# Performance work log

Hardware: AMD Instinct MI355X
Metric: run time of the kernel (lower is better)

The kernel has to match this reference:

```python
import jax, jax.numpy as jnp
import numpy as np

N, F, H, E, ES, G = 50000, 64, 4, 300000, 400000, 128
NS, EPS = 0.2, 1e-5  # LeakyReLU slope, BN eps


def setup_inputs() -> dict:
    k = jax.random.split(jax.random.key(0), 16)
    rn = lambda i, s, sc=1.0: jax.random.normal(k[i], s, jnp.float32) * sc
    return {
        "x": rn(0, (N, F)),
        "edge_index": jax.random.randint(k[1], (2, E), 0, N),
        "batch": jnp.sort(jax.random.randint(k[2], (N,), 0, G)),
        "scatter_edge_index": jax.random.randint(k[3], (4, 2, ES), 0, N),
        "scatter_edge_attr": rn(4, (4, ES), 0.1),
        "gat_W": rn(5, (4, F, H * F), 0.05),
        "gat_asrc": rn(6, (4, H, F), 0.05),
        "gat_adst": rn(7, (4, H, F), 0.05),
        "gat_bias": jnp.zeros((4, H * F)),
        "mlp_W": rn(8, (4, H * F, F), 0.05),
        "mlp_b": jnp.zeros((4, F)),
        "mlp_g": jnp.ones((4, F)), "mlp_beta": jnp.zeros((4, F)),
        "mlp_rm": jnp.zeros((4, F)), "mlp_rv": jax.random.uniform(k[9], (4, F)) + 0.5,
        "fc1_W": rn(10, (F, 256), 0.05), "fc1_b": jnp.zeros((256,)),
        "fc1_g": jnp.ones((256,)), "fc1_beta": jnp.zeros((256,)),
        "fc1_rm": jnp.zeros((256,)), "fc1_rv": jax.random.uniform(k[11], (256,)) + 0.5,
        "fc2_W": rn(12, (256, 64), 0.05), "fc2_b": jnp.zeros((64,)),
        "fc2_g": jnp.ones((64,)), "fc2_beta": jnp.zeros((64,)),
        "fc2_rm": jnp.zeros((64,)), "fc2_rv": jax.random.uniform(k[13], (64,)) + 0.5,
        "fc3_W": rn(14, (64, 10), 0.05), "fc3_b": jnp.zeros((10,)),
        "fc3_g": jnp.ones((10,)), "fc3_beta": jnp.zeros((10,)),
        "fc3_rm": jnp.zeros((10,)), "fc3_rv": jax.random.uniform(k[15], (10,)) + 0.5,
    }


def _bn(h, g, b, rm, rv):
    # BatchNorm1d in eval mode (running stats)
    return g * (h - rm) * jax.lax.rsqrt(rv + EPS) + b


def _forward(floats, ints):
    (x, sea, gW, gas, gad, gb, mW, mb, mg, mbe, mrm, mrv,
     f1W, f1b, f1g, f1be, f1rm, f1rv, f2W, f2b, f2g, f2be, f2rm, f2rv,
     f3W, f3b, f3g, f3be, f3rm, f3rv) = floats
    edge_index, batch, sei = ints
    n = x.shape[0]
    loop = jnp.arange(n)
    src = jnp.concatenate([edge_index[0], loop])  # GATConv adds self-loops
    dst = jnp.concatenate([edge_index[1], loop])

    def solo(i, h):
        # edge_attr-weighted scatter-add (solo_pass, aggr='add')
        s, t = sei[i, 0], sei[i, 1]
        return jax.ops.segment_sum(sea[i][:, None] * h[s], t, num_segments=n)

    def gat_mlp(i, h):
        hh = (h @ gW[i]).reshape(n, H, F)                       # [N,H,F]
        e = (hh * gas[i]).sum(-1)[src] + (hh * gad[i]).sum(-1)[dst]  # [E+N,H]
        e = jnp.where(e > 0, e, NS * e)                         # LeakyReLU(0.2)
        m = jax.ops.segment_max(e, dst, num_segments=n)         # segment softmax over dst
        ex = jnp.exp(e - m[dst])
        ssum = jax.ops.segment_sum(ex, dst, num_segments=n)
        alpha = ex / ssum[dst]
        out = jax.ops.segment_sum(hh[src] * alpha[:, :, None], dst, num_segments=n)
        out = out.reshape(n, H * F) + gb[i]                     # concat heads + bias
        h2 = jax.nn.elu(out) @ mW[i] + mb[i]                    # ELU -> Dropout(eval) -> Linear
        return _bn(h2, mg[i], mbe[i], mrm[i], mrv[i])

    x0 = solo(0, x)
    xh = [jnp.abs(solo(i, x)) for i in (1, 2, 3)]
    branches = [x0] + [solo(0, h) for h in xh]
    branches = [gat_mlp(i, branches[i]) for i in range(4)]
    x_stage2 = x + branches[0] + branches[1] + branches[2] + branches[3]
    pooled = jax.ops.segment_sum(x_stage2, batch, num_segments=G)   # global_add_pool
    h = jax.nn.relu(_bn(pooled @ f1W + f1b, f1g, f1be, f1rm, f1rv))
    h = jax.nn.relu(_bn(h @ f2W + f2b, f2g, f2be, f2rm, f2rv))
    return _bn(h @ f3W + f3b, f3g, f3be, f3rm, f3rv)  # [G, num_classes]


def reference(x, edge_index, batch, scatter_edge_index, scatter_edge_attr, gat_W, gat_asrc, gat_adst, gat_bias, mlp_W, mlp_b, mlp_g, mlp_beta, mlp_rm, mlp_rv, fc1_W, fc1_b, fc1_g, fc1_beta, fc1_rm, fc1_rv, fc2_W, fc2_b, fc2_g, fc2_beta, fc2_rm, fc2_rv, fc3_W, fc3_b, fc3_g, fc3_beta, fc3_rm, fc3_rv):
    floats = (x, scatter_edge_attr, gat_W, gat_asrc, gat_adst, gat_bias, mlp_W, mlp_b, mlp_g, mlp_beta, mlp_rm, mlp_rv, fc1_W, fc1_b, fc1_g, fc1_beta, fc1_rm, fc1_rv, fc2_W, fc2_b, fc2_g, fc2_beta, fc2_rm, fc2_rv, fc3_W, fc3_b, fc3_g, fc3_beta, fc3_rm, fc3_rv)
    return _forward(floats, (edge_index, batch, scatter_edge_index))
```

## Files before the change

kernel.cpp:

```cpp
#include <hip/hip_runtime.h>

typedef unsigned int uint;

#define NN 50000
#define FF 64
#define NHD 4
#define EE 300000
#define ESN 400000
#define NG 128
#define NSLOPE 0.2f
#define EPSBN 1e-5f
#define NTILE 3125

#define BINSZ 64
#define NBIN 782
#define CHUNK 2048
#define NBLK 196
#define BST 40
#define BCAP 38

typedef float f32x4 __attribute__((ext_vector_type(4)));
typedef float f32x2 __attribute__((ext_vector_type(2)));
typedef short bf16x8 __attribute__((ext_vector_type(8)));
union U8 { uint4 u; bf16x8 s; };

static __device__ __forceinline__ float lrelu(float e) {
  return fmaxf(e, NSLOPE * e);
}
static __device__ __forceinline__ float bl(uint u) {
  return __uint_as_float(u << 16);
}
static __device__ __forceinline__ float bh(uint u) {
  return __uint_as_float(u & 0xFFFF0000u);
}
static __device__ __forceinline__ uint f2bf(float f) {
  uint u = __float_as_uint(f);
  return (u + 0x7FFFu + ((u >> 16) & 1u)) >> 16;
}
static __device__ __forceinline__ uint packbf(float a, float b) {
  return f2bf(a) | (f2bf(b) << 16);
}

__global__ __launch_bounds__(256) void k_setup(
    const float2* __restrict__ x, const float* __restrict__ gW,
    const float* __restrict__ gas, const float* __restrict__ gad,
    const float* __restrict__ mW, const float* __restrict__ mb,
    const float* __restrict__ mg, const float* __restrict__ mbe,
    const float* __restrict__ mrm, const float* __restrict__ mrv,
    uint* __restrict__ xbf, uint* __restrict__ WB, uint* __restrict__ SB,
    uint* __restrict__ MB, float* __restrict__ cvec) {
  int i = blockIdx.x * 256 + threadIdx.x;
  if (i < NN * 32) {
    float2 v = x[i];
    xbf[i] = packbf(v.x, v.y);
  }
  int t = i;
  if (t < 8192) {
    int b = t >> 11, rem = t & 2047;
    int tt = rem >> 6, l = rem & 63;
    int tile = tt >> 1, q2 = tt & 1;
    int c = tile * 16 + (l & 15);
    int k0 = q2 * 32 + (l >> 4) * 8;
    const float* Wp = gW + b * 16384;
    uint4 o;
    o.x = packbf(Wp[(k0 + 0) * 256 + c], Wp[(k0 + 1) * 256 + c]);
    o.y = packbf(Wp[(k0 + 2) * 256 + c], Wp[(k0 + 3) * 256 + c]);
    o.z = packbf(Wp[(k0 + 4) * 256 + c], Wp[(k0 + 5) * 256 + c]);
    o.w = packbf(Wp[(k0 + 6) * 256 + c], Wp[(k0 + 7) * 256 + c]);
    ((uint4*)WB)[t] = o;
  } else if (t < 8192 + 2048) {
    int id = t - 8192;
    int b = id >> 9, rem = id & 511;
    int q2 = rem >> 6, l = rem & 63;
    int n = l & 15;
    int k0 = q2 * 32 + (l >> 4) * 8;
    const float* ap = gas + b * 256;
    const float* dp = gad + b * 256;
    float v[8];
#pragma unroll
    for (int j = 0; j < 8; ++j) {
      int c = k0 + j, h = c >> 6, f = c & 63;
      float val = 0.f;
      if (n < 4) val = (h == n) ? ap[n * 64 + f] : 0.f;
      else if (n < 8) val = (h == n - 4) ? dp[(n - 4) * 64 + f] : 0.f;
      v[j] = val;
    }
    uint4 o;
    o.x = packbf(v[0], v[1]); o.y = packbf(v[2], v[3]);
    o.z = packbf(v[4], v[5]); o.w = packbf(v[6], v[7]);
    ((uint4*)SB)[id] = o;
  } else if (t < 8192 + 2048 + 8192) {
    int id = t - 10240;
    int b = id >> 11, rem = id & 2047;
    int tt = rem >> 6, l = rem & 63;
    int tile = tt >> 3, q2 = tt & 7;
    int c = tile * 16 + (l & 15);
    int k0 = q2 * 32 + (l >> 4) * 8;
    const float* Mp = mW + b * 16384;
    float sc = mg[b * 64 + c] * rsqrtf(mrv[b * 64 + c] + EPSBN);
    float v[8];
#pragma unroll
    for (int j = 0; j < 8; ++j) {
      int kp = k0 + j;
      int ko = (kp & 3) * 64 + (kp >> 2);
      v[j] = Mp[ko * 64 + c] * sc;
    }
    uint4 o;
    o.x = packbf(v[0], v[1]); o.y = packbf(v[2], v[3]);
    o.z = packbf(v[4], v[5]); o.w = packbf(v[6], v[7]);
    ((uint4*)MB)[id] = o;
  } else if (t < 8192 + 2048 + 8192 + 64) {
    int c = t - 18432;
    float acc = 0.f;
#pragma unroll
    for (int b = 0; b < 4; ++b) {
      float sc = mg[b * 64 + c] * rsqrtf(mrv[b * 64 + c] + EPSBN);
      acc += sc * (mb[b * 64 + c] - mrm[b * 64 + c]) + mbe[b * 64 + c];
    }
    cvec[c] = acc;
  }
}

__global__ __launch_bounds__(256) void k_sort1(
    const int* __restrict__ sei, const float* __restrict__ sea,
    const int* __restrict__ ei, uint2* __restrict__ sorted,
    unsigned short* __restrict__ offs) {
  __shared__ uint hist[NBIN];
  __shared__ uint wsum[4];
  __shared__ __align__(16) uint2 buf[CHUNK];
  int y = blockIdx.y, blk = blockIdx.x, tid = threadIdx.x;
  int E = (y < 4) ? ESN : EE;
  int e0 = blk * CHUNK;
  if (e0 >= E) return;
  int ec = E - e0; if (ec > CHUNK) ec = CHUNK;
  for (int i = tid; i < NBIN; i += 256) hist[i] = 0;
  __syncthreads();
  const int* sptr; const int* tptr; const float* wptr = 0;
  if (y < 4) {
    sptr = sei + (size_t)y * 2 * ESN; tptr = sptr + ESN;
    wptr = sea + (size_t)y * ESN;
  } else {
    sptr = ei; tptr = ei + EE;
  }
  uint2 rec[8]; uint rbin[8];
#pragma unroll
  for (int k = 0; k < 8; ++k) {
    int idx = tid + k * 256;
    rbin[k] = 0xFFFFFFFFu;
    if (idx < ec) {
      int e = e0 + idx;
      int s = sptr[e], t = tptr[e];
      uint w = (y < 4) ? (f2bf(wptr[e]) << 16) : 0u;
      rec[k].x = (uint)s | ((uint)(t & 63) << 16);
      rec[k].y = w;
      rbin[k] = (uint)(t >> 6);
      atomicAdd(&hist[rbin[k]], 1u);
    }
  }
  __syncthreads();
  int t4 = tid * 4;
  uint h0 = 0, h1 = 0, h2 = 0, h3 = 0;
  if (t4 + 0 < NBIN) h0 = hist[t4 + 0];
  if (t4 + 1 < NBIN) h1 = hist[t4 + 1];
  if (t4 + 2 < NBIN) h2 = hist[t4 + 2];
  if (t4 + 3 < NBIN) h3 = hist[t4 + 3];
  uint sl = h0 + h1 + h2 + h3;
  uint pre = sl;
#pragma unroll
  for (int off = 1; off < 64; off <<= 1) {
    uint nv = __shfl_up(pre, off);
    if ((tid & 63) >= off) pre += nv;
  }
  int wid = tid >> 6;
  if ((tid & 63) == 63) wsum[wid] = pre;
  __syncthreads();
  uint wbase = 0;
#pragma unroll
  for (int w = 0; w < 4; ++w) if (w < wid) wbase += wsum[w];
  uint base = wbase + pre - sl;
  if (t4 + 0 < NBIN) hist[t4 + 0] = base;
  if (t4 + 1 < NBIN) hist[t4 + 1] = base + h0;
  if (t4 + 2 < NBIN) hist[t4 + 2] = base + h0 + h1;
  if (t4 + 3 < NBIN) hist[t4 + 3] = base + h0 + h1 + h2;
  __syncthreads();
  unsigned short* ob = offs + ((size_t)y * NBLK + blk) * 784;
  for (int i = tid; i < NBIN; i += 256) ob[i] = (unsigned short)hist[i];
  if (tid == 0) { ob[NBIN] = (unsigned short)ec; ob[NBIN + 1] = (unsigned short)ec; }
  __syncthreads();
#pragma unroll
  for (int k = 0; k < 8; ++k) {
    if (rbin[k] != 0xFFFFFFFFu) {
      uint p = atomicAdd(&hist[rbin[k]], 1u);
      buf[p] = rec[k];
    }
  }
  __syncthreads();
  uint2* sb = sorted + ((size_t)y * NBLK + blk) * CHUNK;
  uint4* s4 = (uint4*)sb;
  const uint4* b4 = (const uint4*)buf;
  int n4 = (ec + 1) >> 1;
  for (int i = tid; i < n4; i += 256) s4[i] = b4[i];
}

__global__ __launch_bounds__(256) void k_sort2(
    const unsigned short* __restrict__ offs, const uint2* __restrict__ sorted,
    uint* __restrict__ pbk, uint* __restrict__ gbk) {
  __shared__ __align__(16) uint Lb[BINSZ * BST];
  __shared__ uint Lc[BINSZ];
  int y = blockIdx.y, bin = blockIdx.x, tid = threadIdx.x;
  if (tid < BINSZ) Lc[tid] = 0u;
  __syncthreads();
  int nblk = (y < 4) ? NBLK : 147;
  for (int sb = tid; sb < nblk; sb += 256) {
    const unsigned short* ob = offs + ((size_t)y * NBLK + sb) * 784;
    uint st = ob[bin], en = ob[bin + 1];
    const uint2* src = sorted + ((size_t)y * NBLK + sb) * CHUNK;
    for (uint i = st; i < en; ++i) {
      uint2 r = src[i];
      uint tl = (r.x >> 16) & 63u;
      uint p = atomicAdd(&Lc[tl], 1u);
      if (p < BCAP) Lb[tl * BST + 2 + p] = (r.x & 0xFFFFu) | r.y;
    }
  }
  __syncthreads();
  if (tid < BINSZ) Lb[tid * BST] = Lc[tid];
  __syncthreads();
  int n0 = bin * BINSZ;
  int nodes = NN - n0;
  if (nodes > BINSZ) nodes = BINSZ;
  uint* out = (y < 4) ? (pbk + ((size_t)y * NN + n0) * BST)
                      : (gbk + (size_t)n0 * BST);
  int tot4 = nodes * (BST / 4);
  uint4* o4v = (uint4*)out;
  const uint4* L4 = (const uint4*)Lb;
  for (int i = tid; i < tot4; i += 256) o4v[i] = L4[i];
}

__global__ __launch_bounds__(256) void k_solo_gA(
    const uint* __restrict__ xbf, const uint* __restrict__ pbk,
    uint* __restrict__ bbuf, uint* __restrict__ tmpb) {
  int i = blockIdx.y;
  int tid = threadIdx.x;
  int n = blockIdx.x * 32 + (tid >> 3);
  int sl = tid & 7;
  if (n >= NN) return;
  const uint* bk = pbk + ((size_t)i * NN + n) * BST;
  int deg = (int)bk[0]; deg = deg > BCAP ? BCAP : deg;
  const uint* pp = bk + 2;
  f32x2 A0 = {0.f, 0.f}, A1 = {0.f, 0.f}, A2 = {0.f, 0.f}, A3 = {0.f, 0.f};
  f32x2 B0 = {0.f, 0.f}, B1 = {0.f, 0.f}, B2 = {0.f, 0.f}, B3 = {0.f, 0.f};
  for (int j = 0; j < deg; j += 2) {
    uint2 pe2 = *(const uint2*)&pp[j];
    if (j + 1 >= deg) pe2.y = 0u;
    float w0 = bh(pe2.x), w1 = bh(pe2.y);
    f32x2 w20 = {w0, w0}, w21 = {w1, w1};
    uint4 v0 = *(const uint4*)&xbf[(size_t)(pe2.x & 0xFFFFu) * 32 + sl * 4];
    uint4 v1 = *(const uint4*)&xbf[(size_t)(pe2.y & 0xFFFFu) * 32 + sl * 4];
    A0 += (f32x2){bl(v0.x), bh(v0.x)} * w20;
    A1 += (f32x2){bl(v0.y), bh(v0.y)} * w20;
    A2 += (f32x2){bl(v0.z), bh(v0.z)} * w20;
    A3 += (f32x2){bl(v0.w), bh(v0.w)} * w20;
    B0 += (f32x2){bl(v1.x), bh(v1.x)} * w21;
    B1 += (f32x2){bl(v1.y), bh(v1.y)} * w21;
    B2 += (f32x2){bl(v1.z), bh(v1.z)} * w21;
    B3 += (f32x2){bl(v1.w), bh(v1.w)} * w21;
  }
  A0 += B0; A1 += B1; A2 += B2; A3 += B3;
  uint4 o;
  o.x = packbf(A0[0], A0[1]); o.y = packbf(A1[0], A1[1]);
  o.z = packbf(A2[0], A2[1]); o.w = packbf(A3[0], A3[1]);
  uint* out = (i == 0) ? bbuf : (tmpb + (size_t)(i - 1) * NN * 32);
  *(uint4*)&out[(size_t)n * 32 + sl * 4] = o;
}

__global__ __launch_bounds__(256) void k_solo_gB(
    const uint* __restrict__ tmpb, const uint* __restrict__ pbk,
    uint* __restrict__ bbuf) {
  int j0 = blockIdx.y;
  int tid = threadIdx.x;
  int n = blockIdx.x * 32 + (tid >> 3);
  int sl = tid & 7;
  if (n >= NN) return;
  const uint* bk = pbk + (size_t)n * BST;
  int deg = (int)bk[0]; deg = deg > BCAP ? BCAP : deg;
  const uint* pp = bk + 2;
  const uint* tin = tmpb + (size_t)j0 * NN * 32;
  f32x2 A0 = {0.f, 0.f}, A1 = {0.f, 0.f}, A2 = {0.f, 0.f}, A3 = {0.f, 0.f};
  f32x2 B0 = {0.f, 0.f}, B1 = {0.f, 0.f}, B2 = {0.f, 0.f}, B3 = {0.f, 0.f};
  for (int j = 0; j < deg; j += 2) {
    uint2 pe2 = *(const uint2*)&pp[j];
    if (j + 1 >= deg) pe2.y = 0u;
    float w0 = bh(pe2.x), w1 = bh(pe2.y);
    f32x2 w20 = {w0, w0}, w21 = {w1, w1};
    uint4 v0 = *(const uint4*)&tin[(size_t)(pe2.x & 0xFFFFu) * 32 + sl * 4];
    uint4 v1 = *(const uint4*)&tin[(size_t)(pe2.y & 0xFFFFu) * 32 + sl * 4];
    A0 += (f32x2){fabsf(bl(v0.x)), fabsf(bh(v0.x))} * w20;
    A1 += (f32x2){fabsf(bl(v0.y)), fabsf(bh(v0.y))} * w20;
    A2 += (f32x2){fabsf(bl(v0.z)), fabsf(bh(v0.z))} * w20;
    A3 += (f32x2){fabsf(bl(v0.w)), fabsf(bh(v0.w))} * w20;
    B0 += (f32x2){fabsf(bl(v1.x)), fabsf(bh(v1.x))} * w21;
    B1 += (f32x2){fabsf(bl(v1.y)), fabsf(bh(v1.y))} * w21;
    B2 += (f32x2){fabsf(bl(v1.z)), fabsf(bh(v1.z))} * w21;
    B3 += (f32x2){fabsf(bl(v1.w)), fabsf(bh(v1.w))} * w21;
  }
  A0 += B0; A1 += B1; A2 += B2; A3 += B3;
  uint4 o;
  o.x = packbf(A0[0], A0[1]); o.y = packbf(A1[0], A1[1]);
  o.z = packbf(A2[0], A2[1]); o.w = packbf(A3[0], A3[1]);
  *(uint4*)&bbuf[(size_t)(j0 + 1) * NN * 32 + (size_t)n * 32 + sl * 4] = o;
}

#define GST 260
__global__ __launch_bounds__(256) void k_gemm_all(
    const uint* __restrict__ bbuf, const uint* __restrict__ WB4,
    const uint* __restrict__ SB4, uint* __restrict__ hh4,
    float* __restrict__ es4, float* __restrict__ ed4) {
  __shared__ float lds[4][16 * GST];
  int b = blockIdx.y;
  const uint* bbuf_i = bbuf + (size_t)b * NN * 32;
  const uint4* WBb = (const uint4*)WB4 + b * 2048;
  const uint4* SBb = (const uint4*)SB4 + b * 512;
  uint* hh = hh4 + (size_t)b * NN * 128;
  float* es = es4 + (size_t)b * NN * 4;
  float* ed = ed4 + (size_t)b * NN * 4;
  int tid = threadIdx.x, wv = tid >> 6, l = tid & 63;
  int quad = l >> 4, m = l & 15;
  int tile = blockIdx.x * 4 + wv;
  if (tile >= NTILE) return;
  int base = tile * 16;
  U8 B[32];
#pragma unroll
  for (int tt = 0; tt < 32; ++tt) B[tt].u = WBb[tt * 64 + l];
  U8 S[8];
#pragma unroll
  for (int q2 = 0; q2 < 8; ++q2) S[q2].u = SBb[q2 * 64 + l];
  U8 a0, a1;
  a0.u = *(const uint4*)&bbuf_i[(size_t)(base + m) * 32 + quad * 4];
  a1.u = *(const uint4*)&bbuf_i[(size_t)(base + m) * 32 + 16 + quad * 4];
  float* L = lds[wv];
#pragma unroll
  for (int t = 0; t < 16; ++t) {
    f32x4 acc = {0.f, 0.f, 0.f, 0.f};
    acc = __builtin_amdgcn_mfma_f32_16x16x32_bf16(a0.s, B[t * 2].s, acc, 0, 0, 0);
    acc = __builtin_amdgcn_mfma_f32_16x16x32_bf16(a1.s, B[t * 2 + 1].s, acc, 0, 0, 0);
#pragma unroll
    for (int r = 0; r < 4; ++r) L[(quad * 4 + r) * GST + t * 16 + m] = acc[r];
  }
  f32x4 accS = {0.f, 0.f, 0.f, 0.f};
#pragma unroll
  for (int q2 = 0; q2 < 8; ++q2) {
    int k0 = q2 * 32 + quad * 8;
    float4 lo = *(const float4*)&L[m * GST + k0];
    float4 hi = *(const float4*)&L[m * GST + k0 + 4];
    U8 af;
    af.u.x = packbf(lo.x, lo.y); af.u.y = packbf(lo.z, lo.w);
    af.u.z = packbf(hi.x, hi.y); af.u.w = packbf(hi.z, hi.w);
    accS = __builtin_amdgcn_mfma_f32_16x16x32_bf16(af.s, S[q2].s, accS, 0, 0, 0);
  }
#pragma unroll
  for (int r = 0; r < 4; ++r) {
    int node = base + quad * 4 + r;
    if (m < 4) es[node * 4 + m] = accS[r];
    else if (m < 8) ed[node * 4 + (m - 4)] = accS[r];
  }
  for (int n = 0; n < 16; ++n) {
    float v0 = L[n * GST + l];
    float v1 = L[n * GST + 64 + l];
    float v2 = L[n * GST + 128 + l];
    float v3 = L[n * GST + 192 + l];
    uint2 o;
    o.x = packbf(v0, v1); o.y = packbf(v2, v3);
    *(uint2*)&hh[(size_t)(base + n) * 128 + l * 2] = o;
  }
}

__global__ __launch_bounds__(256) void k_attn_all(
    const uint* __restrict__ gbk, const float* __restrict__ es4,
    const float* __restrict__ ed4, const uint* __restrict__ hh4,
    const float* __restrict__ gb, uint* __restrict__ att4) {
  __shared__ uint4 meta[4][2][32];
  int b = blockIdx.y;
  const float4* es44 = (const float4*)(es4 + (size_t)b * NN * 4);
  const float4* ed44 = (const float4*)(ed4 + (size_t)b * NN * 4);
  const char* hhB = (const char*)(hh4 + (size_t)b * NN * 128);
  const float* gbb = gb + b * 256;
  uint* att = att4 + (size_t)b * NN * 128;
  int wv = threadIdx.x >> 6, lane = threadIdx.x & 63;
  int half = lane >> 5, hl = lane & 31;
  int d = blockIdx.x * 8 + wv * 2 + half;
  int deg = (int)gbk[(size_t)d * BST]; deg = deg > 31 ? 31 : deg;
  float4 edd = ed44[d];
  bool act = hl <= deg;
  int s0 = d;
  if (hl < deg) s0 = (int)gbk[(size_t)d * BST + 2 + hl];
  float4 e4 = es44[s0];
  float val[4];
  val[0] = act ? lrelu(e4.x + edd.x) : -3e38f;
  val[1] = act ? lrelu(e4.y + edd.y) : -3e38f;
  val[2] = act ? lrelu(e4.z + edd.z) : -3e38f;
  val[3] = act ? lrelu(e4.w + edd.w) : -3e38f;
  float m[4] = {val[0], val[1], val[2], val[3]};
#pragma unroll
  for (int off = 1; off < 32; off <<= 1)
#pragma unroll
    for (int h = 0; h < 4; ++h) m[h] = fmaxf(m[h], __shfl_xor(m[h], off));
  float e[4], sm[4];
#pragma unroll
  for (int h = 0; h < 4; ++h) {
    e[h] = act ? __expf(val[h] - m[h]) : 0.f;
    sm[h] = e[h];
  }
#pragma unroll
  for (int off = 1; off < 32; off <<= 1)
#pragma unroll
    for (int h = 0; h < 4; ++h) sm[h] += __shfl_xor(sm[h], off);
  meta[wv][half][hl] =
      make_uint4((uint)s0 * 512u, packbf(e[0] / sm[0], e[1] / sm[1]),
                 packbf(e[2] / sm[2], e[3] / sm[3]), 0u);
  int tot = deg + 1;
  f32x2 A0 = {0.f, 0.f}, A1 = {0.f, 0.f}, A2 = {0.f, 0.f}, A3 = {0.f, 0.f};
  f32x2 B0 = {0.f, 0.f}, B1 = {0.f, 0.f}, B2 = {0.f, 0.f}, B3 = {0.f, 0.f};
  int passes = (tot + 1) >> 1;
  for (int p = 0; p < passes; ++p) {
    uint4 ma = meta[wv][half][2 * p];
    uint4 mb_ = meta[wv][half][2 * p + 1];
    uint4 r0 = *(const uint4*)(hhB + ma.x + hl * 16);
    uint4 r1 = *(const uint4*)(hhB + mb_.x + hl * 16);
    f32x2 wA0 = {bl(ma.y), bh(ma.y)}, wB0 = {bl(ma.z), bh(ma.z)};
    f32x2 wA1 = {bl(mb_.y), bh(mb_.y)}, wB1 = {bl(mb_.z), bh(mb_.z)};
    A0 += (f32x2){bl(r0.x), bh(r0.x)} * wA0;
    A1 += (f32x2){bl(r0.y), bh(r0.y)} * wB0;
    A2 += (f32x2){bl(r0.z), bh(r0.z)} * wA0;
    A3 += (f32x2){bl(r0.w), bh(r0.w)} * wB0;
    B0 += (f32x2){bl(r1.x), bh(r1.x)} * wA1;
    B1 += (f32x2){bl(r1.y), bh(r1.y)} * wB1;
    B2 += (f32x2){bl(r1.z), bh(r1.z)} * wA1;
    B3 += (f32x2){bl(r1.w), bh(r1.w)} * wB1;
  }
  A0 += B0; A1 += B1; A2 += B2; A3 += B3;
  float ov[8] = {A0[0], A0[1], A1[0], A1[1], A2[0], A2[1], A3[0], A3[1]};
#pragma unroll
  for (int k = 0; k < 8; ++k) {
    float g = gbb[(k & 3) * 64 + hl * 2 + (k >> 2)];
    float v = ov[k] + g;
    ov[k] = v > 0.f ? v : (__expf(v) - 1.f);
  }
  uint4 o;
  o.x = packbf(ov[0], ov[1]); o.y = packbf(ov[2], ov[3]);
  o.z = packbf(ov[4], ov[5]); o.w = packbf(ov[6], ov[7]);
  *(uint4*)&att[(size_t)d * 128 + hl * 4] = o;
}

#define MST 68
__global__ __launch_bounds__(256) void k_mlp_all(
    const uint* __restrict__ att4, const uint* __restrict__ MB4,
    const float* __restrict__ cvec, const float* __restrict__ xsrc,
    float* __restrict__ xs2) {
  __shared__ float lds[4][16 * MST];
  int tid = threadIdx.x, wv = tid >> 6, l = tid & 63;
  int quad = l >> 4, m = l & 15;
  int tile = blockIdx.x * 4 + wv;
  if (tile >= NTILE) return;
  int base = tile * 16;
  f32x4 acc[4] = {{0.f, 0.f, 0.f, 0.f},
                  {0.f, 0.f, 0.f, 0.f},
                  {0.f, 0.f, 0.f, 0.f},
                  {0.f, 0.f, 0.f, 0.f}};
  for (int b = 0; b < 4; ++b) {
    const uint4* MBb = (const uint4*)MB4 + b * 2048;
    const uint* att = att4 + (size_t)b * NN * 128;
    U8 B[32];
#pragma unroll
    for (int tt = 0; tt < 32; ++tt) B[tt].u = MBb[tt * 64 + l];
    U8 A[8];
#pragma unroll
    for (int q2 = 0; q2 < 8; ++q2)
      A[q2].u =
          *(const uint4*)&att[(size_t)(base + m) * 128 + q2 * 16 + quad * 4];
#pragma unroll
    for (int t = 0; t < 4; ++t)
#pragma unroll
      for (int q2 = 0; q2 < 8; ++q2)
        acc[t] = __builtin_amdgcn_mfma_f32_16x16x32_bf16(A[q2].s,
                                                         B[t * 8 + q2].s,
                                                         acc[t], 0, 0, 0);
  }
  float* L = lds[wv];
#pragma unroll
  for (int t = 0; t < 4; ++t)
#pragma unroll
    for (int r = 0; r < 4; ++r) L[(quad * 4 + r) * MST + t * 16 + m] = acc[t][r];
  float cv = cvec[l];
  for (int n = 0; n < 16; ++n) {
    float v = L[n * MST + l];
    size_t idx = (size_t)(base + n) * 64 + l;
    xs2[idx] = xsrc[idx] + v + cv;
  }
}

__global__ __launch_bounds__(256) void k_poolhead(
    const float* __restrict__ xs2, const int* __restrict__ batch,
    const float* __restrict__ f1W, const float* __restrict__ f1b,
    const float* __restrict__ f1g, const float* __restrict__ f1be,
    const float* __restrict__ f1rm, const float* __restrict__ f1rv,
    const float* __restrict__ f2W, const float* __restrict__ f2b,
    const float* __restrict__ f2g, const float* __restrict__ f2be,
    const float* __restrict__ f2rm, const float* __restrict__ f2rv,
    const float* __restrict__ f3W, const float* __restrict__ f3b,
    const float* __restrict__ f3g, const float* __restrict__ f3be,
    const float* __restrict__ f3rm, const float* __restrict__ f3rv,
    float* __restrict__ out) {
  __shared__ float p[64], h1[256], h2[64], red[4][64];
  int g = blockIdx.x, tid = threadIdx.x;
  int wv = tid >> 6, lane = tid & 63;
  int lo = 0, hi = NN;
  while (lo < hi) { int mid = (lo + hi) >> 1; if (batch[mid] < g) lo = mid + 1; else hi = mid; }
  int beg = lo;
  lo = 0; hi = NN;
  while (lo < hi) { int mid = (lo + hi) >> 1; if (batch[mid] < g + 1) lo = mid + 1; else hi = mid; }
  int end = lo;
  float acc = 0.f;
  for (int n = beg + wv; n < end; n += 4) acc += xs2[(size_t)n * FF + lane];
  red[wv][lane] = acc;
  __syncthreads();
  if (tid < 64) p[tid] = red[0][tid] + red[1][tid] + red[2][tid] + red[3][tid];
  __syncthreads();
  {
    float a = f1b[tid];
    for (int k = 0; k < 64; ++k) a += p[k] * f1W[k * 256 + tid];
// ... 26 lines not shown
  const float* sea   = (const float*)d_in[4];
  const float* gW    = (const float*)d_in[5];
  const float* gas   = (const float*)d_in[6];
  const float* gad   = (const float*)d_in[7];
  const float* gb    = (const float*)d_in[8];
  const float* mW    = (const float*)d_in[9];
  const float* mb    = (const float*)d_in[10];
  const float* mg    = (const float*)d_in[11];
  const float* mbe   = (const float*)d_in[12];
  const float* mrm   = (const float*)d_in[13];
  const float* mrv   = (const float*)d_in[14];
  const float* f1W   = (const float*)d_in[15];
  const float* f1b   = (const float*)d_in[16];
  const float* f1g   = (const float*)d_in[17];
  const float* f1be  = (const float*)d_in[18];
  const float* f1rm  = (const float*)d_in[19];
  const float* f1rv  = (const float*)d_in[20];
  const float* f2W   = (const float*)d_in[21];
  const float* f2b   = (const float*)d_in[22];
  const float* f2g   = (const float*)d_in[23];
  const float* f2be  = (const float*)d_in[24];
  const float* f2rm  = (const float*)d_in[25];
  const float* f2rv  = (const float*)d_in[26];
  const float* f3W   = (const float*)d_in[27];
  const float* f3b   = (const float*)d_in[28];
  const float* f3g   = (const float*)d_in[29];
  const float* f3be  = (const float*)d_in[30];
  const float* f3rm  = (const float*)d_in[31];
  const float* f3rv  = (const float*)d_in[32];
  float* out = (float*)d_out;

  char* base = (char*)d_ws;
  float* xs2 = (float*)base;
  uint* gbk  = (uint*)base;
  uint* xbf  = (uint*)(base + (size_t)NN * 64 * 4);
  uint* bbuf = xbf + (size_t)NN * 32;
  uint* hh4  = bbuf + (size_t)4 * NN * 32;
  uint* tmpb = hh4;
  uint2* sorted = (uint2*)(hh4 + (size_t)3 * NN * 32);
  unsigned short* offs =
      (unsigned short*)(sorted + (size_t)5 * NBLK * CHUNK);
  uint* att4 = hh4 + (size_t)4 * NN * 128;
  uint* pbk  = att4;
  float* es4 = (float*)(att4 + (size_t)4 * NN * 128);
  float* ed4 = es4 + (size_t)4 * NN * 4;
  float* cvec = ed4 + (size_t)4 * NN * 4;
  uint* WB4 = (uint*)(cvec + 64);
  uint* SB4 = WB4 + 4 * 8192;
  uint* MB4 = SB4 + 4 * 2048;

  size_t need = (size_t)((char*)(MB4 + 4 * 8192) - base);
  if (ws_size < need) return;

  k_setup<<<(NN * 32 + 255) / 256, 256, 0, stream>>>(
      (const float2*)x, gW, gas, gad, mW, mb, mg, mbe, mrm, mrv, xbf, WB4,
      SB4, MB4, cvec);

  dim3 gS1(NBLK, 5);
  k_sort1<<<gS1, 256, 0, stream>>>(sei, sea, ei, sorted, offs);
  dim3 gS2(NBIN, 5);
  k_sort2<<<gS2, 256, 0, stream>>>(offs, sorted, pbk, gbk);

  dim3 gA((NN + 31) / 32, 4);
  k_solo_gA<<<gA, 256, 0, stream>>>(xbf, pbk, bbuf, tmpb);
  dim3 gB((NN + 31) / 32, 3);
  k_solo_gB<<<gB, 256, 0, stream>>>(tmpb, pbk, bbuf);

  const int gT = (NTILE + 3) / 4;
  dim3 gG(gT, 4);
  k_gemm_all<<<gG, 256, 0, stream>>>(bbuf, WB4, SB4, hh4, es4, ed4);
  dim3 gAt(NN / 8, 4);
  k_attn_all<<<gAt, 256, 0, stream>>>(gbk, es4, ed4, hh4, gb, att4);
  k_mlp_all<<<gT, 256, 0, stream>>>(att4, MB4, cvec, x, xs2);

  k_poolhead<<<NG, 256, 0, stream>>>(xs2, batch, f1W, f1b, f1g, f1be, f1rm,
                                     f1rv, f2W, f2b, f2g, f2be, f2rm, f2rv,
                                     f3W, f3b, f3g, f3be, f3rm, f3rv, out);
}
```

Measured before the change: 459.1 us.

## Aggregate before projection in GAT and fuse attention, projection and MLP into one kernel

```diff
diff --git a/kernel.cpp b/kernel.cpp
--- a/kernel.cpp
+++ b/kernel.cpp
@@ -1,6 +1,7 @@
 #include <hip/hip_runtime.h>
 
 typedef unsigned int uint;
+typedef unsigned short u16;
 
 #define NN 50000
 #define FF 64
@@ -10,7 +11,6 @@
 #define NG 128
 #define NSLOPE 0.2f
 #define EPSBN 1e-5f
-#define NTILE 3125
 
 #define BINSZ 64
 #define NBIN 782
@@ -47,7 +47,7 @@
     const float* __restrict__ mW, const float* __restrict__ mb,
     const float* __restrict__ mg, const float* __restrict__ mbe,
     const float* __restrict__ mrm, const float* __restrict__ mrv,
-    uint* __restrict__ xbf, uint* __restrict__ WB, uint* __restrict__ SB,
+    uint* __restrict__ xbf, uint* __restrict__ WB2, float* __restrict__ wasd,
     uint* __restrict__ MB, float* __restrict__ cvec) {
   int i = blockIdx.x * 256 + threadIdx.x;
   if (i < NN * 32) {
@@ -56,10 +56,11 @@
   }
   int t = i;
   if (t < 8192) {
-    int b = t >> 11, rem = t & 2047;
-    int tt = rem >> 6, l = rem & 63;
-    int tile = tt >> 1, q2 = tt & 1;
-    int c = tile * 16 + (l & 15);
+    int b = t >> 11, id = t & 2047;
+    int h = id >> 9, r2 = id & 511;
+    int q2 = r2 >> 8, r3 = r2 & 255;
+    int ct = r3 >> 6, l = r3 & 63;
+    int c = h * 64 + ct * 16 + (l & 15);
     int k0 = q2 * 32 + (l >> 4) * 8;
     const float* Wp = gW + b * 16384;
     uint4 o;
@@ -67,28 +68,17 @@
     o.y = packbf(Wp[(k0 + 2) * 256 + c], Wp[(k0 + 3) * 256 + c]);
     o.z = packbf(Wp[(k0 + 4) * 256 + c], Wp[(k0 + 5) * 256 + c]);
     o.w = packbf(Wp[(k0 + 6) * 256 + c], Wp[(k0 + 7) * 256 + c]);
-    ((uint4*)WB)[t] = o;
+    ((uint4*)WB2)[t] = o;
   } else if (t < 8192 + 2048) {
     int id = t - 8192;
-    int b = id >> 9, rem = id & 511;
-    int q2 = rem >> 6, l = rem & 63;
-    int n = l & 15;
-    int k0 = q2 * 32 + (l >> 4) * 8;
-    const float* ap = gas + b * 256;
-    const float* dp = gad + b * 256;
-    float v[8];
-#pragma unroll
-    for (int j = 0; j < 8; ++j) {
-      int c = k0 + j, h = c >> 6, f = c & 63;
-      float val = 0.f;
-      if (n < 4) val = (h == n) ? ap[n * 64 + f] : 0.f;
-      else if (n < 8) val = (h == n - 4) ? dp[(n - 4) * 64 + f] : 0.f;
-      v[j] = val;
-    }
-    uint4 o;
-    o.x = packbf(v[0], v[1]); o.y = packbf(v[2], v[3]);
-    o.z = packbf(v[4], v[5]); o.w = packbf(v[6], v[7]);
-    ((uint4*)SB)[id] = o;
+    int b = id >> 9, r = id & 511;
+    int sd = r >> 8, r2 = r & 255;
+    int h = r2 >> 6, k = r2 & 63;
+    const float* Wp = gW + b * 16384;
+    const float* ap = (sd ? gad : gas) + b * 256 + h * 64;
+    float acc = 0.f;
+    for (int f = 0; f < 64; ++f) acc += Wp[k * 256 + h * 64 + f] * ap[f];
+    wasd[((b * 2 + sd) * 4 + h) * 64 + k] = acc;
   } else if (t < 8192 + 2048 + 8192) {
     int id = t - 10240;
     int b = id >> 11, rem = id & 2047;
@@ -100,11 +90,7 @@
     float sc = mg[b * 64 + c] * rsqrtf(mrv[b * 64 + c] + EPSBN);
     float v[8];
 #pragma unroll
-    for (int j = 0; j < 8; ++j) {
-      int kp = k0 + j;
-      int ko = (kp & 3) * 64 + (kp >> 2);
-      v[j] = Mp[ko * 64 + c] * sc;
-    }
+    for (int j = 0; j < 8; ++j) v[j] = Mp[(k0 + j) * 64 + c] * sc;
     uint4 o;
     o.x = packbf(v[0], v[1]); o.y = packbf(v[2], v[3]);
     o.z = packbf(v[4], v[5]); o.w = packbf(v[6], v[7]);
@@ -124,7 +110,7 @@
 __global__ __launch_bounds__(256) void k_sort1(
     const int* __restrict__ sei, const float* __restrict__ sea,
     const int* __restrict__ ei, uint2* __restrict__ sorted,
-    unsigned short* __restrict__ offs) {
+    u16* __restrict__ offs) {
   __shared__ uint hist[NBIN];
   __shared__ uint wsum[4];
   __shared__ __align__(16) uint2 buf[CHUNK];
@@ -183,9 +169,9 @@
   if (t4 + 2 < NBIN) hist[t4 + 2] = base + h0 + h1;
   if (t4 + 3 < NBIN) hist[t4 + 3] = base + h0 + h1 + h2;
   __syncthreads();
-  unsigned short* ob = offs + ((size_t)y * NBLK + blk) * 784;
-  for (int i = tid; i < NBIN; i += 256) ob[i] = (unsigned short)hist[i];
-  if (tid == 0) { ob[NBIN] = (unsigned short)ec; ob[NBIN + 1] = (unsigned short)ec; }
+  u16* ob = offs + ((size_t)y * NBLK + blk) * 784;
+  for (int i = tid; i < NBIN; i += 256) ob[i] = (u16)hist[i];
+  if (tid == 0) { ob[NBIN] = (u16)ec; ob[NBIN + 1] = (u16)ec; }
   __syncthreads();
 #pragma unroll
   for (int k = 0; k < 8; ++k) {
@@ -203,7 +189,7 @@
 }
 
 __global__ __launch_bounds__(256) void k_sort2(
-    const unsigned short* __restrict__ offs, const uint2* __restrict__ sorted,
+    const u16* __restrict__ offs, const uint2* __restrict__ sorted,
     uint* __restrict__ pbk, uint* __restrict__ gbk) {
   __shared__ __align__(16) uint Lb[BINSZ * BST];
   __shared__ uint Lc[BINSZ];
@@ -212,7 +198,7 @@
   __syncthreads();
   int nblk = (y < 4) ? NBLK : 147;
   for (int sb = tid; sb < nblk; sb += 256) {
-    const unsigned short* ob = offs + ((size_t)y * NBLK + sb) * 784;
+    const u16* ob = offs + ((size_t)y * NBLK + sb) * 784;
     uint st = ob[bin], en = ob[bin + 1];
     const uint2* src = sorted + ((size_t)y * NBLK + sb) * CHUNK;
     for (uint i = st; i < en; ++i) {
@@ -238,7 +224,9 @@
 
 __global__ __launch_bounds__(256) void k_solo_gA(
     const uint* __restrict__ xbf, const uint* __restrict__ pbk,
-    uint* __restrict__ bbuf, uint* __restrict__ tmpb) {
+    const float* __restrict__ wasd, uint* __restrict__ bbuf,
+    uint* __restrict__ tmpb, float* __restrict__ es4,
+    float* __restrict__ ed4) {
   int i = blockIdx.y;
   int tid = threadIdx.x;
   int n = blockIdx.x * 32 + (tid >> 3);
@@ -271,12 +259,35 @@
   o.z = packbf(A2[0], A2[1]); o.w = packbf(A3[0], A3[1]);
   uint* out = (i == 0) ? bbuf : (tmpb + (size_t)(i - 1) * NN * 32);
   *(uint4*)&out[(size_t)n * 32 + sl * 4] = o;
+  if (i == 0) {
+    float pv[8] = {A0[0], A0[1], A1[0], A1[1], A2[0], A2[1], A3[0], A3[1]};
+    const float* wa = wasd;
+    float r[8];
+#pragma unroll
+    for (int o8 = 0; o8 < 8; ++o8) {
+      const float* w8 = wa + o8 * 64 + sl * 8;
+      float a = 0.f;
+#pragma unroll
+      for (int j = 0; j < 8; ++j) a += pv[j] * w8[j];
+      r[o8] = a;
+    }
+#pragma unroll
+    for (int off = 1; off < 8; off <<= 1)
+#pragma unroll
+      for (int o8 = 0; o8 < 8; ++o8) r[o8] += __shfl_xor(r[o8], off);
+    if (sl == 0) {
+      *(float4*)&es4[(size_t)n * 4] = make_float4(r[0], r[1], r[2], r[3]);
+      *(float4*)&ed4[(size_t)n * 4] = make_float4(r[4], r[5], r[6], r[7]);
+    }
+  }
 }
 
 __global__ __launch_bounds__(256) void k_solo_gB(
     const uint* __restrict__ tmpb, const uint* __restrict__ pbk,
-    uint* __restrict__ bbuf) {
+    const float* __restrict__ wasd, uint* __restrict__ bbuf,
+    float* __restrict__ es4, float* __restrict__ ed4) {
   int j0 = blockIdx.y;
+  int b = j0 + 1;
   int tid = threadIdx.x;
   int n = blockIdx.x * 32 + (tid >> 3);
   int sl = tid & 7;
@@ -307,194 +318,220 @@
   uint4 o;
   o.x = packbf(A0[0], A0[1]); o.y = packbf(A1[0], A1[1]);
   o.z = packbf(A2[0], A2[1]); o.w = packbf(A3[0], A3[1]);
-  *(uint4*)&bbuf[(size_t)(j0 + 1) * NN * 32 + (size_t)n * 32 + sl * 4] = o;
-}
-
-#define GST 260
-__global__ __launch_bounds__(256) void k_gemm_all(
-    const uint* __restrict__ bbuf, const uint* __restrict__ WB4,
-    const uint* __restrict__ SB4, uint* __restrict__ hh4,
-    float* __restrict__ es4, float* __restrict__ ed4) {
-  __shared__ float lds[4][16 * GST];
-  int b = blockIdx.y;
-  const uint* bbuf_i = bbuf + (size_t)b * NN * 32;
-  const uint4* WBb = (const uint4*)WB4 + b * 2048;
-  const uint4* SBb = (const uint4*)SB4 + b * 512;
-  uint* hh = hh4 + (size_t)b * NN * 128;
-  float* es = es4 + (size_t)b * NN * 4;
-  float* ed = ed4 + (size_t)b * NN * 4;
-  int tid = threadIdx.x, wv = tid >> 6, l = tid & 63;
-  int quad = l >> 4, m = l & 15;
-  int tile = blockIdx.x * 4 + wv;
-  if (tile >= NTILE) return;
-  int base = tile * 16;
-  U8 B[32];
-#pragma unroll
-  for (int tt = 0; tt < 32; ++tt) B[tt].u = WBb[tt * 64 + l];
-  U8 S[8];
-#pragma unroll
-  for (int q2 = 0; q2 < 8; ++q2) S[q2].u = SBb[q2 * 64 + l];
-  U8 a0, a1;
-  a0.u = *(const uint4*)&bbuf_i[(size_t)(base + m) * 32 + quad * 4];
-  a1.u = *(const uint4*)&bbuf_i[(size_t)(base + m) * 32 + 16 + quad * 4];
-  float* L = lds[wv];
-#pragma unroll
-  for (int t = 0; t < 16; ++t) {
-    f32x4 acc = {0.f, 0.f, 0.f, 0.f};
-    acc = __builtin_amdgcn_mfma_f32_16x16x32_bf16(a0.s, B[t * 2].s, acc, 0, 0, 0);
-    acc = __builtin_amdgcn_mfma_f32_16x16x32_bf16(a1.s, B[t * 2 + 1].s, acc, 0, 0, 0);
-#pragma unroll
-    for (int r = 0; r < 4; ++r) L[(quad * 4 + r) * GST + t * 16 + m] = acc[r];
-  }
-  f32x4 accS = {0.f, 0.f, 0.f, 0.f};
-#pragma unroll
-  for (int q2 = 0; q2 < 8; ++q2) {
-    int k0 = q2 * 32 + quad * 8;
-    float4 lo = *(const float4*)&L[m * GST + k0];
-    float4 hi = *(const float4*)&L[m * GST + k0 + 4];
-    U8 af;
-    af.u.x = packbf(lo.x, lo.y); af.u.y = packbf(lo.z, lo.w);
-    af.u.z = packbf(hi.x, hi.y); af.u.w = packbf(hi.z, hi.w);
-    accS = __builtin_amdgcn_mfma_f32_16x16x32_bf16(af.s, S[q2].s, accS, 0, 0, 0);
-  }
-#pragma unroll
-  for (int r = 0; r < 4; ++r) {
-    int node = base + quad * 4 + r;
-    if (m < 4) es[node * 4 + m] = accS[r];
-    else if (m < 8) ed[node * 4 + (m - 4)] = accS[r];
-  }
-  for (int n = 0; n < 16; ++n) {
-    float v0 = L[n * GST + l];
-    float v1 = L[n * GST + 64 + l];
-    float v2 = L[n * GST + 128 + l];
-    float v3 = L[n * GST + 192 + l];
-    uint2 o;
-    o.x = packbf(v0, v1); o.y = packbf(v2, v3);
-    *(uint2*)&hh[(size_t)(base + n) * 128 + l * 2] = o;
-  }
-}
-
-__global__ __launch_bounds__(256) void k_attn_all(
+  *(uint4*)&bbuf[(size_t)b * NN * 32 + (size_t)n * 32 + sl * 4] = o;
+  {
+    float pv[8] = {A0[0], A0[1], A1[0], A1[1], A2[0], A2[1], A3[0], A3[1]};
+    const float* wa = wasd + b * 512;
+    float r[8];
+#pragma unroll
+    for (int o8 = 0; o8 < 8; ++o8) {
+      const float* w8 = wa + o8 * 64 + sl * 8;
+      float a = 0.f;
+#pragma unroll
+      for (int j = 0; j < 8; ++j) a += pv[j] * w8[j];
+      r[o8] = a;
+    }
+#pragma unroll
+    for (int off = 1; off < 8; off <<= 1)
+#pragma unroll
+      for (int o8 = 0; o8 < 8; ++o8) r[o8] += __shfl_xor(r[o8], off);
+    if (sl == 0) {
+      *(float4*)&es4[(size_t)b * NN * 4 + (size_t)n * 4] =
+          make_float4(r[0], r[1], r[2], r[3]);
+      *(float4*)&ed4[(size_t)b * NN * 4 + (size_t)n * 4] =
+          make_float4(r[4], r[5], r[6], r[7]);
+    }
+  }
+}
+
+__global__ __launch_bounds__(256) void k_fuse(
     const uint* __restrict__ gbk, const float* __restrict__ es4,
-    const float* __restrict__ ed4, const uint* __restrict__ hh4,
-    const float* __restrict__ gb, uint* __restrict__ att4) {
-  __shared__ uint4 meta[4][2][32];
-  int b = blockIdx.y;
-  const float4* es44 = (const float4*)(es4 + (size_t)b * NN * 4);
-  const float4* ed44 = (const float4*)(ed4 + (size_t)b * NN * 4);
-  const char* hhB = (const char*)(hh4 + (size_t)b * NN * 128);
-  const float* gbb = gb + b * 256;
-  uint* att = att4 + (size_t)b * NN * 128;
-  int wv = threadIdx.x >> 6, lane = threadIdx.x & 63;
-  int half = lane >> 5, hl = lane & 31;
-  int d = blockIdx.x * 8 + wv * 2 + half;
-  int deg = (int)gbk[(size_t)d * BST]; deg = deg > 31 ? 31 : deg;
-  float4 edd = ed44[d];
-  bool act = hl <= deg;
-  int s0 = d;
-  if (hl < deg) s0 = (int)gbk[(size_t)d * BST + 2 + hl];
-  float4 e4 = es44[s0];
-  float val[4];
-  val[0] = act ? lrelu(e4.x + edd.x) : -3e38f;
-  val[1] = act ? lrelu(e4.y + edd.y) : -3e38f;
-  val[2] = act ? lrelu(e4.z + edd.z) : -3e38f;
-  val[3] = act ? lrelu(e4.w + edd.w) : -3e38f;
-  float m[4] = {val[0], val[1], val[2], val[3]};
-#pragma unroll
-  for (int off = 1; off < 32; off <<= 1)
-#pragma unroll
-    for (int h = 0; h < 4; ++h) m[h] = fmaxf(m[h], __shfl_xor(m[h], off));
-  float e[4], sm[4];
-#pragma unroll
-  for (int h = 0; h < 4; ++h) {
-    e[h] = act ? __expf(val[h] - m[h]) : 0.f;
-    sm[h] = e[h];
-  }
-#pragma unroll
-  for (int off = 1; off < 32; off <<= 1)
-#pragma unroll
-    for (int h = 0; h < 4; ++h) sm[h] += __shfl_xor(sm[h], off);
-  meta[wv][half][hl] =
-      make_uint4((uint)s0 * 512u, packbf(e[0] / sm[0], e[1] / sm[1]),
-                 packbf(e[2] / sm[2], e[3] / sm[3]), 0u);
-  int tot = deg + 1;
-  f32x2 A0 = {0.f, 0.f}, A1 = {0.f, 0.f}, A2 = {0.f, 0.f}, A3 = {0.f, 0.f};
-  f32x2 B0 = {0.f, 0.f}, B1 = {0.f, 0.f}, B2 = {0.f, 0.f}, B3 = {0.f, 0.f};
-  int passes = (tot + 1) >> 1;
-  for (int p = 0; p < passes; ++p) {
-    uint4 ma = meta[wv][half][2 * p];
-    uint4 mb_ = meta[wv][half][2 * p + 1];
-    uint4 r0 = *(const uint4*)(hhB + ma.x + hl * 16);
-    uint4 r1 = *(const uint4*)(hhB + mb_.x + hl * 16);
-    f32x2 wA0 = {bl(ma.y), bh(ma.y)}, wB0 = {bl(ma.z), bh(ma.z)};
-    f32x2 wA1 = {bl(mb_.y), bh(mb_.y)}, wB1 = {bl(mb_.z), bh(mb_.z)};
-    A0 += (f32x2){bl(r0.x), bh(r0.x)} * wA0;
-    A1 += (f32x2){bl(r0.y), bh(r0.y)} * wB0;
-    A2 += (f32x2){bl(r0.z), bh(r0.z)} * wA0;
-    A3 += (f32x2){bl(r0.w), bh(r0.w)} * wB0;
-    B0 += (f32x2){bl(r1.x), bh(r1.x)} * wA1;
-    B1 += (f32x2){bl(r1.y), bh(r1.y)} * wB1;
-    B2 += (f32x2){bl(r1.z), bh(r1.z)} * wA1;
-    B3 += (f32x2){bl(r1.w), bh(r1.w)} * wB1;
-  }
-  A0 += B0; A1 += B1; A2 += B2; A3 += B3;
-  float ov[8] = {A0[0], A0[1], A1[0], A1[1], A2[0], A2[1], A3[0], A3[1]};
-#pragma unroll
-  for (int k = 0; k < 8; ++k) {
-    float g = gbb[(k & 3) * 64 + hl * 2 + (k >> 2)];
-    float v = ov[k] + g;
-    ov[k] = v > 0.f ? v : (__expf(v) - 1.f);
-  }
-  uint4 o;
-  o.x = packbf(ov[0], ov[1]); o.y = packbf(ov[2], ov[3]);
-  o.z = packbf(ov[4], ov[5]); o.w = packbf(ov[6], ov[7]);
-  *(uint4*)&att[(size_t)d * 128 + hl * 4] = o;
-}
-
-#define MST 68
-__global__ __launch_bounds__(256) void k_mlp_all(
-    const uint* __restrict__ att4, const uint* __restrict__ MB4,
-    const float* __restrict__ cvec, const float* __restrict__ xsrc,
-    float* __restrict__ xs2) {
-  __shared__ float lds[4][16 * MST];
-  int tid = threadIdx.x, wv = tid >> 6, l = tid & 63;
-  int quad = l >> 4, m = l & 15;
-  int tile = blockIdx.x * 4 + wv;
-  if (tile >= NTILE) return;
-  int base = tile * 16;
-  f32x4 acc[4] = {{0.f, 0.f, 0.f, 0.f},
-                  {0.f, 0.f, 0.f, 0.f},
-                  {0.f, 0.f, 0.f, 0.f},
-                  {0.f, 0.f, 0.f, 0.f}};
+    const float* __restrict__ ed4, const uint* __restrict__ bbuf,
+    const uint* __restrict__ WB2, const uint* __restrict__ MB4,
+    const float* __restrict__ gb, const float* __restrict__ cvec,
+    const float* __restrict__ xsrc, float* __restrict__ xs2) {
+  __shared__ uint gbr[32][40];
+  __shared__ uint2 meta[32][32];
+  __shared__ union UU {
+    struct { uint agg[32][128]; u16 elu[4][32][64]; } s;
+    float red[4][32][64];
+  } u;
+  int tid = threadIdx.x;
+  int n0 = blockIdx.x * 32;
+  int wv = tid >> 6, l = tid & 63;
+  int quad = l >> 4, m16 = l & 15;
+
+  for (int idx = tid; idx < 320; idx += 256) {
+    int i = idx / 10, q = idx % 10;
+    int nd = n0 + i;
+    uint4 v = (nd < NN) ? *(const uint4*)&gbk[(size_t)nd * BST + q * 4]
+                        : make_uint4(0, 0, 0, 0);
+    *(uint4*)&gbr[i][q * 4] = v;
+  }
+  __syncthreads();
+
+  f32x4 macc[2][4];
+#pragma unroll
+  for (int a = 0; a < 2; ++a)
+#pragma unroll
+    for (int c = 0; c < 4; ++c) macc[a][c] = (f32x4){0.f, 0.f, 0.f, 0.f};
+
   for (int b = 0; b < 4; ++b) {
-    const uint4* MBb = (const uint4*)MB4 + b * 2048;
-    const uint* att = att4 + (size_t)b * NN * 128;
-    U8 B[32];
-#pragma unroll
-    for (int tt = 0; tt < 32; ++tt) B[tt].u = MBb[tt * 64 + l];
-    U8 A[8];
-#pragma unroll
-    for (int q2 = 0; q2 < 8; ++q2)
-      A[q2].u =
-          *(const uint4*)&att[(size_t)(base + m) * 128 + q2 * 16 + quad * 4];
+    const float4* es44 = (const float4*)(es4 + (size_t)b * NN * 4);
+    const float4* ed44 = (const float4*)(ed4 + (size_t)b * NN * 4);
+    const uint* bbf = bbuf + (size_t)b * NN * 32;
+    {
+      int g = tid >> 5, hl = tid & 31;
+#pragma unroll
+      for (int rep = 0; rep < 4; ++rep) {
+        int i = rep * 8 + g;
+        int nd = n0 + i;
+        bool vld = nd < NN;
+        int nds = vld ? nd : 0;
+        int deg = vld ? (int)gbr[i][0] : 0;
+        deg = deg > 31 ? 31 : deg;
+        int s0 = (hl < deg) ? (int)gbr[i][2 + hl] : nds;
+        bool act = hl <= deg;
+        float4 edd = ed44[nds];
+        float4 e4 = es44[s0];
+        float val[4];
+        val[0] = act ? lrelu(e4.x + edd.x) : -3e38f;
+        val[1] = act ? lrelu(e4.y + edd.y) : -3e38f;
+        val[2] = act ? lrelu(e4.z + edd.z) : -3e38f;
+        val[3] = act ? lrelu(e4.w + edd.w) : -3e38f;
+        float m[4] = {val[0], val[1], val[2], val[3]};
+#pragma unroll
+        for (int off = 1; off < 32; off <<= 1)
+#pragma unroll
+          for (int h = 0; h < 4; ++h) m[h] = fmaxf(m[h], __shfl_xor(m[h], off));
+        float e[4], sm[4];
+#pragma unroll
+        for (int h = 0; h < 4; ++h) {
+          e[h] = act ? __expf(val[h] - m[h]) : 0.f;
+          sm[h] = e[h];
+        }
+#pragma unroll
+        for (int off = 1; off < 32; off <<= 1)
+#pragma unroll
+          for (int h = 0; h < 4; ++h) sm[h] += __shfl_xor(sm[h], off);
+        meta[i][hl] = make_uint2(packbf(e[0] / sm[0], e[1] / sm[1]),
+                                 packbf(e[2] / sm[2], e[3] / sm[3]));
+      }
+    }
+    __syncthreads();
+    {
+      int i = wv * 8 + (l >> 3), sl = l & 7;
+      int nd = n0 + i;
+      bool vld = nd < NN;
+      int self = vld ? nd : 0;
+      int deg = vld ? (int)gbr[i][0] : 0;
+      deg = deg > 31 ? 31 : deg;
+      int tot = deg + 1;
+      f32x2 ag00 = {0.f, 0.f}, ag01 = {0.f, 0.f}, ag02 = {0.f, 0.f}, ag03 = {0.f, 0.f};
+      f32x2 ag10 = {0.f, 0.f}, ag11 = {0.f, 0.f}, ag12 = {0.f, 0.f}, ag13 = {0.f, 0.f};
+      f32x2 ag20 = {0.f, 0.f}, ag21 = {0.f, 0.f}, ag22 = {0.f, 0.f}, ag23 = {0.f, 0.f};
+      f32x2 ag30 = {0.f, 0.f}, ag31 = {0.f, 0.f}, ag32 = {0.f, 0.f}, ag33 = {0.f, 0.f};
+      for (int j = 0; j < tot; ++j) {
+        int src = (j < deg) ? (int)gbr[i][2 + j] : self;
+        uint2 al = meta[i][j];
+        uint4 v = *(const uint4*)&bbf[(size_t)src * 32 + sl * 4];
+        f32x2 w0 = {bl(al.x), bl(al.x)}, w1 = {bh(al.x), bh(al.x)};
+        f32x2 w2 = {bl(al.y), bl(al.y)}, w3 = {bh(al.y), bh(al.y)};
+        f32x2 v0 = {bl(v.x), bh(v.x)}, v1 = {bl(v.y), bh(v.y)};
+        f32x2 v2 = {bl(v.z), bh(v.z)}, v3 = {bl(v.w), bh(v.w)};
+        ag00 += v0 * w0; ag01 += v1 * w0; ag02 += v2 * w0; ag03 += v3 * w0;
+        ag10 += v0 * w1; ag11 += v1 * w1; ag12 += v2 * w1; ag13 += v3 * w1;
+        ag20 += v0 * w2; ag21 += v1 * w2; ag22 += v2 * w2; ag23 += v3 * w2;
+        ag30 += v0 * w3; ag31 += v1 * w3; ag32 += v2 * w3; ag33 += v3 * w3;
+      }
+      uint4 o;
+      o.x = packbf(ag00[0], ag00[1]); o.y = packbf(ag01[0], ag01[1]);
+      o.z = packbf(ag02[0], ag02[1]); o.w = packbf(ag03[0], ag03[1]);
+      *(uint4*)&u.s.agg[i][0 * 32 + sl * 4] = o;
+      o.x = packbf(ag10[0], ag10[1]); o.y = packbf(ag11[0], ag11[1]);
+      o.z = packbf(ag12[0], ag12[1]); o.w = packbf(ag13[0], ag13[1]);
+      *(uint4*)&u.s.agg[i][1 * 32 + sl * 4] = o;
+      o.x = packbf(ag20[0], ag20[1]); o.y = packbf(ag21[0], ag21[1]);
+      o.z = packbf(ag22[0], ag22[1]); o.w = packbf(ag23[0], ag23[1]);
+      *(uint4*)&u.s.agg[i][2 * 32 + sl * 4] = o;
+      o.x = packbf(ag30[0], ag30[1]); o.y = packbf(ag31[0], ag31[1]);
+      o.z = packbf(ag32[0], ag32[1]); o.w = packbf(ag33[0], ag33[1]);
+      *(uint4*)&u.s.agg[i][3 * 32 + sl * 4] = o;
+    }
+    __syncthreads();
+    {
+      int h = wv;
+      uint4 Bh[2][4];
+#pragma unroll
+      for (int kk = 0; kk < 2; ++kk)
+#pragma unroll
+        for (int ct = 0; ct < 4; ++ct)
+          Bh[kk][ct] =
+              ((const uint4*)WB2)[(((b * 4 + h) * 2 + kk) * 4 + ct) * 64 + l];
+#pragma unroll
+      for (int mt = 0; mt < 2; ++mt) {
+        U8 a0, a1;
+        a0.u = *(const uint4*)&u.s.agg[mt * 16 + m16][h * 32 + quad * 4];
+        a1.u = *(const uint4*)&u.s.agg[mt * 16 + m16][h * 32 + 16 + quad * 4];
+#pragma unroll
+        for (int ct = 0; ct < 4; ++ct) {
+          f32x4 acc = {0.f, 0.f, 0.f, 0.f};
+          U8 b0, b1; b0.u = Bh[0][ct]; b1.u = Bh[1][ct];
+          acc = __builtin_amdgcn_mfma_f32_16x16x32_bf16(a0.s, b0.s, acc, 0, 0, 0);
+          acc = __builtin_amdgcn_mfma_f32_16x16x32_bf16(a1.s, b1.s, acc, 0, 0, 0);
+          float gbv = gb[b * 256 + h * 64 + ct * 16 + m16];
+#pragma unroll
+          for (int r = 0; r < 4; ++r) {
+            float v = acc[r] + gbv;
+            v = v > 0.f ? v : (__expf(v) - 1.f);
+            u.s.elu[wv][mt * 16 + quad * 4 + r][ct * 16 + m16] = (u16)f2bf(v);
+          }
+        }
+      }
+    }
+    {
+      const uint4* MBb = (const uint4*)MB4 + b * 2048;
+      uint4 Bm[4][2];
+#pragma unroll
+      for (int t = 0; t < 4; ++t)
+#pragma unroll
+        for (int kk = 0; kk < 2; ++kk)
+          Bm[t][kk] = MBb[(t * 8 + wv * 2 + kk) * 64 + l];
+      const uint* ew = (const uint*)&u.s.elu[wv][0][0];
+#pragma unroll
+      for (int mt = 0; mt < 2; ++mt) {
+        U8 a0, a1;
+        a0.u = *(const uint4*)&ew[(mt * 16 + m16) * 32 + quad * 4];
+        a1.u = *(const uint4*)&ew[(mt * 16 + m16) * 32 + 16 + quad * 4];
+#pragma unroll
+        for (int t = 0; t < 4; ++t) {
+          U8 b0, b1; b0.u = Bm[t][0]; b1.u = Bm[t][1];
+          macc[mt][t] =
+              __builtin_amdgcn_mfma_f32_16x16x32_bf16(a0.s, b0.s, macc[mt][t], 0, 0, 0);
+          macc[mt][t] =
+              __builtin_amdgcn_mfma_f32_16x16x32_bf16(a1.s, b1.s, macc[mt][t], 0, 0, 0);
+        }
+      }
+    }
+    __syncthreads();
+  }
+#pragma unroll
+  for (int mt = 0; mt < 2; ++mt)
 #pragma unroll
     for (int t = 0; t < 4; ++t)
 #pragma unroll
-      for (int q2 = 0; q2 < 8; ++q2)
-        acc[t] = __builtin_amdgcn_mfma_f32_16x16x32_bf16(A[q2].s,
-                                                         B[t * 8 + q2].s,
-                                                         acc[t], 0, 0, 0);
-  }
-  float* L = lds[wv];
-#pragma unroll
-  for (int t = 0; t < 4; ++t)
-#pragma unroll
-    for (int r = 0; r < 4; ++r) L[(quad * 4 + r) * MST + t * 16 + m] = acc[t][r];
-  float cv = cvec[l];
-  for (int n = 0; n < 16; ++n) {
-    float v = L[n * MST + l];
-    size_t idx = (size_t)(base + n) * 64 + l;
-    xs2[idx] = xsrc[idx] + v + cv;
+      for (int r = 0; r < 4; ++r)
+        u.red[wv][mt * 16 + quad * 4 + r][t * 16 + m16] = macc[mt][t][r];
+  __syncthreads();
+  for (int e = tid; e < 2048; e += 256) {
+    int node = e >> 6, col = e & 63;
+    int nd = n0 + node;
+    if (nd < NN) {
+      float v = u.red[0][node][col] + u.red[1][node][col] +
+                u.red[2][node][col] + u.red[3][node][col];
+      size_t idx = (size_t)nd * 64 + col;
+      xs2[idx] = xsrc[idx] + v + cvec[col];
+    }
   }
 }
 
@@ -587,29 +624,26 @@
 
   char* base = (char*)d_ws;
   float* xs2 = (float*)base;
-  uint* gbk  = (uint*)base;
-  uint* xbf  = (uint*)(base + (size_t)NN * 64 * 4);
+  uint* gbk  = (uint*)(base + (size_t)NN * 64 * 4);
+  uint* xbf  = gbk + (size_t)NN * BST;
   uint* bbuf = xbf + (size_t)NN * 32;
-  uint* hh4  = bbuf + (size_t)4 * NN * 32;
-  uint* tmpb = hh4;
-  uint2* sorted = (uint2*)(hh4 + (size_t)3 * NN * 32);
-  unsigned short* offs =
-      (unsigned short*)(sorted + (size_t)5 * NBLK * CHUNK);
-  uint* att4 = hh4 + (size_t)4 * NN * 128;
-  uint* pbk  = att4;
-  float* es4 = (float*)(att4 + (size_t)4 * NN * 128);
+  uint* tmpb = bbuf + (size_t)4 * NN * 32;
+  uint* pbk  = tmpb + (size_t)3 * NN * 32;
+  uint2* sorted = (uint2*)(pbk + (size_t)4 * NN * BST);
+  u16* offs = (u16*)(sorted + (size_t)5 * NBLK * CHUNK);
+  float* es4 = (float*)(offs + (size_t)5 * NBLK * 784);
   float* ed4 = es4 + (size_t)4 * NN * 4;
   float* cvec = ed4 + (size_t)4 * NN * 4;
-  uint* WB4 = (uint*)(cvec + 64);
-  uint* SB4 = WB4 + 4 * 8192;
-  uint* MB4 = SB4 + 4 * 2048;
+  float* wasd = cvec + 64;
+  uint* WB2 = (uint*)(wasd + 2048);
+  uint* MB4 = WB2 + 4 * 8192;
 
   size_t need = (size_t)((char*)(MB4 + 4 * 8192) - base);
   if (ws_size < need) return;
 
   k_setup<<<(NN * 32 + 255) / 256, 256, 0, stream>>>(
-      (const float2*)x, gW, gas, gad, mW, mb, mg, mbe, mrm, mrv, xbf, WB4,
-      SB4, MB4, cvec);
+      (const float2*)x, gW, gas, gad, mW, mb, mg, mbe, mrm, mrv, xbf, WB2,
+      wasd, MB4, cvec);
 
   dim3 gS1(NBLK, 5);
   k_sort1<<<gS1, 256, 0, stream>>>(sei, sea, ei, sorted, offs);
@@ -617,16 +651,12 @@
   k_sort2<<<gS2, 256, 0, stream>>>(offs, sorted, pbk, gbk);
 
   dim3 gA((NN + 31) / 32, 4);
-  k_solo_gA<<<gA, 256, 0, stream>>>(xbf, pbk, bbuf, tmpb);
+  k_solo_gA<<<gA, 256, 0, stream>>>(xbf, pbk, wasd, bbuf, tmpb, es4, ed4);
   dim3 gB((NN + 31) / 32, 3);
-  k_solo_gB<<<gB, 256, 0, stream>>>(tmpb, pbk, bbuf);
-
-  const int gT = (NTILE + 3) / 4;
-  dim3 gG(gT, 4);
-  k_gemm_all<<<gG, 256, 0, stream>>>(bbuf, WB4, SB4, hh4, es4, ed4);
-  dim3 gAt(NN / 8, 4);
-  k_attn_all<<<gAt, 256, 0, stream>>>(gbk, es4, ed4, hh4, gb, att4);
-  k_mlp_all<<<gT, 256, 0, stream>>>(att4, MB4, cvec, x, xs2);
+  k_solo_gB<<<gB, 256, 0, stream>>>(tmpb, pbk, wasd, bbuf, es4, ed4);
+
+  k_fuse<<<(NN + 31) / 32, 256, 0, stream>>>(gbk, es4, ed4, bbuf, WB2, MB4,
+                                             gb, cvec, x, xs2);
 
   k_poolhead<<<NG, 256, 0, stream>>>(xs2, batch, f1W, f1b, f1g, f1be, f1rm,
                                      f1rv, f2W, f2b, f2g, f2be, f2rm, f2rv,
```

Measured after the change: 446.7 us. -2.7%, faster.
